# Kernel tuning notes

Hardware: AMD Instinct MI355X
Metric: run time of the kernel (lower is better)

## Reference

```python
import jax, jax.numpy as jnp
import numpy as np

B, S, H = 1024, 100, 256
C_TANH = 10.0
NEG = -100000.0


def _lin(k, o, i):
    s = 1.0 / np.sqrt(i)
    kw, kb = jax.random.split(k)
    return (jax.random.uniform(kw, (o, i), jnp.float32, -s, s),
            jax.random.uniform(kb, (o,), jnp.float32, -s, s))


def setup_inputs() -> dict:
    key = jax.random.key(0)
    ks = jax.random.split(key, 16)
    inputs = jax.random.uniform(ks[0], (B, S, 2), jnp.float32)
    emb_w, emb_b = _lin(ks[1], H, 2)
    s = 1.0 / np.sqrt(H)
    def lstm(k):
        k1, k2, k3, k4 = jax.random.split(k, 4)
        return (jax.random.uniform(k1, (4 * H, H), jnp.float32, -s, s),
                jax.random.uniform(k2, (4 * H, H), jnp.float32, -s, s),
                jax.random.uniform(k3, (4 * H,), jnp.float32, -s, s),
                jax.random.uniform(k4, (4 * H,), jnp.float32, -s, s))
    enc_wih, enc_whh, enc_bih, enc_bhh = lstm(ks[2])
    dec_wih, dec_whh, dec_bih, dec_bhh = lstm(ks[3])
    ptr_wq_w, ptr_wq_b = _lin(ks[4], H, H)
    ptr_wref_w, ptr_wref_b = _lin(ks[5], H, H)
    ptr_v_w, ptr_v_b = _lin(ks[6], 1, H)
    glm_wq_w, glm_wq_b = _lin(ks[7], H, H)
    glm_wref_w, glm_wref_b = _lin(ks[8], H, H)
    glm_v_w, glm_v_b = _lin(ks[9], 1, H)
    start = jax.random.uniform(ks[10], (H,), jnp.float32, -s, s)
    return dict(inputs=inputs, emb_w=emb_w, emb_b=emb_b,
                enc_wih=enc_wih, enc_whh=enc_whh, enc_bih=enc_bih, enc_bhh=enc_bhh,
                dec_wih=dec_wih, dec_whh=dec_whh, dec_bih=dec_bih, dec_bhh=dec_bhh,
                ptr_wq_w=ptr_wq_w, ptr_wq_b=ptr_wq_b, ptr_wref_w=ptr_wref_w, ptr_wref_b=ptr_wref_b,
                ptr_v_w=ptr_v_w, ptr_v_b=ptr_v_b,
                glm_wq_w=glm_wq_w, glm_wq_b=glm_wq_b, glm_wref_w=glm_wref_w, glm_wref_b=glm_wref_b,
                glm_v_w=glm_v_w, glm_v_b=glm_v_b, start=start)


def _lstm_cell(x, h, c, wih, whh, bih, bhh):
    g = x @ wih.T + bih + h @ whh.T + bhh
    i, f, gg, o = jnp.split(g, 4, axis=-1)  # torch gate order i,f,g,o
    c = jax.nn.sigmoid(f) * c + jax.nn.sigmoid(i) * jnp.tanh(gg)
    h = jax.nn.sigmoid(o) * jnp.tanh(c)
    return h, c


def _attn_logits(q, ref_proj, mask, wq_w, wq_b, v_w, v_b):
    # ref_proj = W_ref(encoder_outputs), precomputed: [B,S,H]
    u = jnp.tanh(ref_proj + (q @ wq_w.T + wq_b)[:, None, :])
    logits = jnp.einsum('bsh,h->bs', u, v_w[0]) + v_b[0]
    logits = jnp.where(mask, NEG, logits)
    return C_TANH * jnp.tanh(logits)


def reference(inputs, emb_w, emb_b,
              enc_wih, enc_whh, enc_bih, enc_bhh,
              dec_wih, dec_whh, dec_bih, dec_bhh,
              ptr_wq_w, ptr_wq_b, ptr_wref_w, ptr_wref_b, ptr_v_w, ptr_v_b,
              glm_wq_w, glm_wq_b, glm_wref_w, glm_wref_b, glm_v_w, glm_v_b,
              start):
    Bn, Sn = inputs.shape[0], inputs.shape[1]
    embedded = inputs @ emb_w.T + emb_b  # [B,S,H]

    def enc_step(carry, x):
        h, c = carry
        h, c = _lstm_cell(x, h, c, enc_wih, enc_whh, enc_bih, enc_bhh)
        return (h, c), h
    z = jnp.zeros((Bn, H), inputs.dtype)
    (h, c), enc_out = jax.lax.scan(enc_step, (z, z), jnp.swapaxes(embedded, 0, 1))
    enc_out = jnp.swapaxes(enc_out, 0, 1)  # [B,S,H]

    ref_g = enc_out @ glm_wref_w.T + glm_wref_b
    ref_p = enc_out @ ptr_wref_w.T + ptr_wref_b
    bidx = jnp.arange(Bn)

    def dec_step(carry, k):
        h, c, mask, dec_in = carry
        h, c = _lstm_cell(dec_in, h, c, dec_wih, dec_whh, dec_bih, dec_bhh)
        q = h
        gl = _attn_logits(q, ref_g, mask, glm_wq_w, glm_wq_b, glm_v_w, glm_v_b)
        q = jnp.einsum('bsh,bs->bh', enc_out, jax.nn.softmax(gl, axis=-1))
        pl = _attn_logits(q, ref_p, mask, ptr_wq_w, ptr_wq_b, ptr_v_w, ptr_v_b)
        logp = jax.nn.log_softmax(pl, axis=-1)
        chosen = jax.random.categorical(k, pl, axis=-1)  # [B]
        lp = jnp.take_along_axis(logp, chosen[:, None], axis=1)[:, 0]
        mask = mask.at[bidx, chosen].set(True)
        dec_in = embedded[bidx, chosen]
        return (h, c, mask, dec_in), (lp, chosen)

    mask0 = jnp.zeros((Bn, Sn), bool)
    dec_in0 = jnp.broadcast_to(start, (Bn, H))
    keys = jax.random.split(jax.random.key(42), Sn)
    _, (lps, chs) = jax.lax.scan(dec_step, (h, c, mask0, dec_in0), keys)
    return jnp.swapaxes(lps, 0, 1), jnp.swapaxes(chs, 0, 1)
```

## Files before the change

kernel.cpp:

```cpp
#include <hip/hip_runtime.h>
#include <cstdint>
#include <cstddef>

#define BB 1024
#define SS 100
#define HH 256

__device__ __forceinline__ unsigned rotl32(unsigned v, int r) {
  return (v << r) | (v >> (32 - r));
}

__device__ __forceinline__ void threefry2x32(unsigned k0, unsigned k1,
                                             unsigned x0, unsigned x1,
                                             unsigned& o0, unsigned& o1) {
  unsigned k2 = k0 ^ k1 ^ 0x1BD11BDAu;
  x0 += k0; x1 += k1;
#define TF_R(r) { x0 += x1; x1 = rotl32(x1, (r)); x1 ^= x0; }
  TF_R(13) TF_R(15) TF_R(26) TF_R(6)
  x0 += k1; x1 += k2 + 1u;
  TF_R(17) TF_R(29) TF_R(16) TF_R(24)
  x0 += k2; x1 += k0 + 2u;
  TF_R(13) TF_R(15) TF_R(26) TF_R(6)
  x0 += k0; x1 += k1 + 3u;
  TF_R(17) TF_R(29) TF_R(16) TF_R(24)
  x0 += k1; x1 += k2 + 4u;
  TF_R(13) TF_R(15) TF_R(26) TF_R(6)
  x0 += k2; x1 += k0 + 5u;
#undef TF_R
  o0 = x0; o1 = x1;
}

__device__ __forceinline__ double sigd(double x) {
  return 1.0 / (1.0 + exp(-x));
}

__device__ __forceinline__ float tanh_fast(float x) {
  float e = __expf(2.0f * x);
  return 1.0f - 2.0f * __builtin_amdgcn_rcpf(e + 1.0f);
}

__device__ __forceinline__ double wave_max(double v) {
#pragma unroll
  for (int off = 32; off; off >>= 1) v = fmax(v, __shfl_xor(v, off));
  return v;
}
__device__ __forceinline__ double wave_sum(double v) {
#pragma unroll
  for (int off = 32; off; off >>= 1) v += __shfl_xor(v, off);
  return v;
}

__global__ __launch_bounds__(256) void init_chunk(
    double* __restrict__ h, double* __restrict__ c) {
  int i = blockIdx.x * 256 + threadIdx.x;
  h[i] = 0.0;
  c[i] = 0.0;
}

__global__ __launch_bounds__(256) void precompute_P(
    const float* __restrict__ emb_w, const float* __restrict__ emb_b,
    const float* __restrict__ start,
    const float* __restrict__ enc_wih, const float* __restrict__ dec_wih,
    double* __restrict__ P) {
  int idx = blockIdx.x * 256 + threadIdx.x;
  int v = idx >> 10, n = idx & 1023;
  const float* W = (v < 3) ? enc_wih : dec_wih;
  int cm = (v < 6) ? (v % 3) : 3;
  const float* wr = W + (size_t)n * HH;
  double acc = 0.0;
  for (int k = 0; k < HH; ++k) {
    double cv;
    if (cm == 0)      cv = (double)emb_w[2 * k];
    else if (cm == 1) cv = (double)emb_w[2 * k + 1];
    else if (cm == 2) cv = (double)emb_b[k];
    else              cv = (double)start[k];
    acc = fma(cv, (double)wr[k], acc);
  }
  P[idx] = acc;
}

__global__ __launch_bounds__(256) void init_dec(
    double* __restrict__ gih, int* __restrict__ mask,
    const double* __restrict__ gih0) {
  const int r = blockIdx.x, t = threadIdx.x;
  if (t < SS) mask[r * SS + t] = 0;
#pragma unroll
  for (int jj = 0; jj < 4; ++jj)
    gih[(size_t)r * 1024 + jj * 256 + t] = gih0[jj * 256 + t];
}

__global__ __launch_bounds__(256) void transpose2(
    const float* __restrict__ a, const float* __restrict__ b,
    float* __restrict__ at, float* __restrict__ bt) {
  int k = blockIdx.x, t = threadIdx.x;
  at[k * HH + t] = a[t * HH + k];
  bt[k * HH + t] = b[t * HH + k];
}

template <bool EMBED>
__global__ __launch_bounds__(256) void lstm_gates(
    const float* __restrict__ inputs, int t, int cb,
    const double* __restrict__ gih,
    const double* __restrict__ Pe,
    const float* __restrict__ Whh,
    const float* __restrict__ bih, const float* __restrict__ bhh,
    const double* __restrict__ hprev, double* __restrict__ hnew,
    double* __restrict__ c, float* __restrict__ enc_c) {
  __shared__ double As[16][34];
  __shared__ double Ws[16][66];
  const int tid = threadIdx.x;
  const int tx = tid & 15;
  const int ty = tid >> 4;
  const int m0 = blockIdx.x * 32;
  const int u0 = blockIdx.y * 16;
  const int arow = tid >> 3;
  const int acol = (tid & 7) * 2;
  const int wn   = tid >> 2;
  const int wcol = (tid & 3) * 4;
  const int wgate = wn >> 4, wu = wn & 15;
  double acc[2][4];

  if (EMBED) {
#pragma unroll
    for (int i = 0; i < 2; ++i) {
      int bb = cb + m0 + ty * 2 + i;
      double i0 = (double)inputs[(bb * SS + t) * 2];
      double i1 = (double)inputs[(bb * SS + t) * 2 + 1];
#pragma unroll
      for (int j = 0; j < 4; ++j) {
        int n = j * 256 + u0 + tx;
        acc[i][j] = fma(i0, Pe[n], fma(i1, Pe[1024 + n], Pe[2048 + n]));
      }
    }
  } else {
#pragma unroll
    for (int i = 0; i < 2; ++i) {
      const double* gr = gih + (size_t)(m0 + ty * 2 + i) * 1024 + u0 + tx;
#pragma unroll
      for (int j = 0; j < 4; ++j) acc[i][j] = gr[j * 256];
    }
  }

  const float* wrow_hh = Whh + (size_t)(wgate * HH + u0 + wu) * HH;

  auto load_slab = [&](int s, double& a0, double& a1, float4& wv) {
    const int k0 = s * 16;
    const double* ar = hprev + (size_t)(m0 + arow) * HH + k0 + acol;
    a0 = ar[0]; a1 = ar[1];
    wv = *(const float4*)(wrow_hh + k0 + wcol);
  };

  double a0c, a1c; float4 wvc;
  load_slab(0, a0c, a1c, wvc);
  for (int s = 0; s < 16; ++s) {
    __syncthreads();
    As[acol][arow] = a0c;
    As[acol + 1][arow] = a1c;
    Ws[wcol + 0][wn] = (double)wvc.x;
    Ws[wcol + 1][wn] = (double)wvc.y;
    Ws[wcol + 2][wn] = (double)wvc.z;
    Ws[wcol + 3][wn] = (double)wvc.w;
    __syncthreads();
    if (s < 15) load_slab(s + 1, a0c, a1c, wvc);
#pragma unroll
    for (int kk = 0; kk < 16; ++kk) {
      double a0k = As[kk][ty * 2];
      double a1k = As[kk][ty * 2 + 1];
#pragma unroll
      for (int j = 0; j < 4; ++j) {
        double w = Ws[kk][j * 16 + tx];
        acc[0][j] = fma(a0k, w, acc[0][j]);
        acc[1][j] = fma(a1k, w, acc[1][j]);
      }
    }
  }

  const int u = u0 + tx;
#pragma unroll
  for (int i = 0; i < 2; ++i) {
    int r = m0 + ty * 2 + i;
    double gi = acc[i][0] + (double)bih[u] + (double)bhh[u];
    double gf = acc[i][1] + (double)bih[HH + u] + (double)bhh[HH + u];
    double gg = acc[i][2] + (double)bih[2 * HH + u] + (double)bhh[2 * HH + u];
    double go = acc[i][3] + (double)bih[3 * HH + u] + (double)bhh[3 * HH + u];
    size_t idx = (size_t)r * HH + u;
    double cp = c[idx];
    double cn = sigd(gf) * cp + sigd(gi) * tanh(gg);
    double hn = sigd(go) * tanh(cn);
    c[idx] = cn;
    hnew[idx] = hn;
    if (enc_c) enc_c[((size_t)r * SS + t) * HH + u] = (float)hn;
  }
}

__global__ __launch_bounds__(256) void proj_gemm(
    const float* __restrict__ A, const float* __restrict__ W,
    const float* __restrict__ bias, float* __restrict__ C) {
  __shared__ double As[16][68];
  __shared__ double Ws[16][68];
  const int tid = threadIdx.x;
  const int tx = tid & 15, ty = tid >> 4;
  const int m0 = blockIdx.x * 64;
  const int n0 = blockIdx.y * 64;
  const int lrow = tid >> 2;
  const int lcol = (tid & 3) << 2;
  double acc[4][4] = {};

  const float* ar = A + (size_t)(m0 + lrow) * HH;
  const float* wr = W + (size_t)(n0 + lrow) * HH;
  for (int k0 = 0; k0 < HH; k0 += 16) {
    float4 av = *(const float4*)(ar + k0 + lcol);
    float4 wv = *(const float4*)(wr + k0 + lcol);
    __syncthreads();
    As[lcol + 0][lrow] = (double)av.x; As[lcol + 1][lrow] = (double)av.y;
    As[lcol + 2][lrow] = (double)av.z; As[lcol + 3][lrow] = (double)av.w;
    Ws[lcol + 0][lrow] = (double)wv.x; Ws[lcol + 1][lrow] = (double)wv.y;
    Ws[lcol + 2][lrow] = (double)wv.z; Ws[lcol + 3][lrow] = (double)wv.w;
    __syncthreads();
#pragma unroll
    for (int kk = 0; kk < 16; ++kk) {
      double a[4], w[4];
#pragma unroll
      for (int i = 0; i < 4; ++i) a[i] = As[kk][ty * 4 + i];
#pragma unroll
      for (int j = 0; j < 4; ++j) w[j] = Ws[kk][tx * 4 + j];
#pragma unroll
      for (int i = 0; i < 4; ++i)
#pragma unroll
        for (int j = 0; j < 4; ++j) acc[i][j] = fma(a[i], w[j], acc[i][j]);
    }
  }
#pragma unroll
  for (int i = 0; i < 4; ++i) {
    float* crow = C + (size_t)(m0 + ty * 4 + i) * HH + n0 + tx * 4;
#pragma unroll
    for (int j = 0; j < 4; ++j)
      crow[j] = (float)(acc[i][j] + (double)bias[n0 + tx * 4 + j]);
  }
}

__global__ __launch_bounds__(256) void dec_attn_sample(
    const double* __restrict__ h,
    const float* __restrict__ enc_c, const float* __restrict__ ref_g,
    const float* __restrict__ ref_p,
    const float* __restrict__ wqt_g, const float* __restrict__ bq_g,
    const float* __restrict__ vw_g, const float* __restrict__ vb_g,
    const float* __restrict__ wqt_p, const float* __restrict__ bq_p,
    const float* __restrict__ vw_p, const float* __restrict__ vb_p,
    int* __restrict__ mask, double* __restrict__ gih,
    const double* __restrict__ Pd,
    const float* __restrict__ inputs,
    float* __restrict__ out, int step, int cb) {
  __shared__ float  hqf[HH];
  __shared__ __align__(16) float qvf[HH];
  __shared__ double lg[SS];
  __shared__ float  lgw[SS];
  __shared__ int    smask[SS];
  __shared__ double redw[4];
  __shared__ int    ridxw[4];
  __shared__ int    sh_chosen;

  const int r = blockIdx.x, t = threadIdx.x;
  const int w = t >> 6, l = t & 63;
  const int b = cb + r;

  hqf[t] = (float)h[(size_t)r * HH + t];
  if (t < SS) smask[t] = mask[r * SS + t];
  __syncthreads();

  {
    float a0 = 0.f, a1 = 0.f, a2 = 0.f, a3 = 0.f;
    for (int k = 0; k < HH; k += 4) {
      a0 = fmaf(wqt_g[(k + 0) * HH + t], hqf[k + 0], a0);
      a1 = fmaf(wqt_g[(k + 1) * HH + t], hqf[k + 1], a1);
      a2 = fmaf(wqt_g[(k + 2) * HH + t], hqf[k + 2], a2);
      a3 = fmaf(wqt_g[(k + 3) * HH + t], hqf[k + 3], a3);
    }
    qvf[t] = ((a0 + a1) + (a2 + a3)) + bq_g[t];
  }
  __syncthreads();

  {
    const float4 vg = *(const float4*)(vw_g + l * 4);
    const float4 qf = *(const float4*)(qvf + l * 4);
    const float vb = vb_g[0];
    for (int s = w; s < SS; s += 4) {
      if (smask[s]) {
        if (l == 0) lg[s] = -10.0;
        continue;
      }
      const float4 rp = *(const float4*)(ref_g + ((size_t)r * SS + s) * HH + l * 4);
      float p = tanh_fast(rp.x + qf.x) * vg.x;
      p = fmaf(tanh_fast(rp.y + qf.y), vg.y, p);
      p = fmaf(tanh_fast(rp.z + qf.z), vg.z, p);
      p = fmaf(tanh_fast(rp.w + qf.w), vg.w, p);
#pragma unroll
      for (int off = 32; off; off >>= 1) p += __shfl_xor(p, off);
      float z = 10.0f * tanh_fast(p + vb);
      if (l == 0) lg[s] = (double)z;
    }
  }
  __syncthreads();

  {
    double x = (t < SS) ? lg[t] : -1e300;
    double vm = wave_max(x);
    if (l == 0) redw[w] = vm;
    __syncthreads();
    double mx = fmax(fmax(redw[0], redw[1]), fmax(redw[2], redw[3]));
    double e = (t < SS) ? exp(x - mx) : 0.0;
    double vs = wave_sum(e);
    __syncthreads();
    if (l == 0) redw[w] = vs;
    __syncthreads();
    double sum = redw[0] + redw[1] + redw[2] + redw[3];
    if (t < SS) lgw[t] = (float)(e / sum);
  }
  __syncthreads();

  {
    const float* eb = enc_c + (size_t)r * SS * HH + t;
    float acc0 = 0.f, acc1 = 0.f, acc2 = 0.f, acc3 = 0.f;
    for (int s = 0; s < SS; s += 4) {
      acc0 = fmaf(eb[(s + 0) * HH], lgw[s + 0], acc0);
      acc1 = fmaf(eb[(s + 1) * HH], lgw[s + 1], acc1);
      acc2 = fmaf(eb[(s + 2) * HH], lgw[s + 2], acc2);
      acc3 = fmaf(eb[(s + 3) * HH], lgw[s + 3], acc3);
    }
    hqf[t] = (acc0 + acc1) + (acc2 + acc3);
  }
  __syncthreads();

  {
    float a0 = 0.f, a1 = 0.f, a2 = 0.f, a3 = 0.f;
    for (int k = 0; k < HH; k += 4) {
      a0 = fmaf(wqt_p[(k + 0) * HH + t], hqf[k + 0], a0);
      a1 = fmaf(wqt_p[(k + 1) * HH + t], hqf[k + 1], a1);
      a2 = fmaf(wqt_p[(k + 2) * HH + t], hqf[k + 2], a2);
      a3 = fmaf(wqt_p[(k + 3) * HH + t], hqf[k + 3], a3);
    }
    qvf[t] = ((a0 + a1) + (a2 + a3)) + bq_p[t];
  }
  __syncthreads();

  {
    const float4 vg = *(const float4*)(vw_p + l * 4);
    const float4 qf = *(const float4*)(qvf + l * 4);
    const float vb = vb_p[0];
    for (int s = w; s < SS; s += 4) {
      if (smask[s]) {
        if (l == 0) lg[s] = -10.0;
        continue;
      }
      const float4 rp = *(const float4*)(ref_p + ((size_t)r * SS + s) * HH + l * 4);
      float p = tanh_fast(rp.x + qf.x) * vg.x;
      p = fmaf(tanh_fast(rp.y + qf.y), vg.y, p);
      p = fmaf(tanh_fast(rp.z + qf.z), vg.z, p);
      p = fmaf(tanh_fast(rp.w + qf.w), vg.w, p);
#pragma unroll
      for (int off = 32; off; off >>= 1) p += __shfl_xor(p, off);
      float z = 10.0f * tanh_fast(p + vb);
      if (l == 0) lg[s] = (double)z;
    }
  }
  __syncthreads();

  double x = (t < SS) ? lg[t] : -1e300;
  double val = -1e300;
  int idx = t;
  if (t < SS) {
    unsigned kk0, kk1;
    threefry2x32(0u, 42u, 0u, (unsigned)step, kk0, kk1);
    unsigned j = (unsigned)(b * SS + t);
    unsigned o0, o1;
    threefry2x32(kk0, kk1, 0u, j, o0, o1);
    unsigned bits = o0 ^ o1;
    double u = (double)(bits >> 9) * 0x1p-23;
    if (u == 0.0) u = 1.17549435e-38;
    val = x + (-log(-log(u)));
  }
#pragma unroll
  for (int off = 32; off; off >>= 1) {
    double v2 = __shfl_xor(val, off);
    int i2 = __shfl_xor(idx, off);
    if (v2 > val || (v2 == val && i2 < idx)) { val = v2; idx = i2; }
  }
  if (l == 0) { redw[w] = val; ridxw[w] = idx; }
  __syncthreads();
  if (t == 0) {
    double bv = redw[0]; int bi = ridxw[0];
#pragma unroll
    for (int i = 1; i < 4; ++i) {
      if (redw[i] > bv || (redw[i] == bv && ridxw[i] < bi)) {
        bv = redw[i]; bi = ridxw[i];
      }
    }
    sh_chosen = bi;
  }
  __syncthreads();
  int chosen = sh_chosen;

  {
    double vm = wave_max(x);
    if (l == 0) redw[w] = vm;
    __syncthreads();
    double mx = fmax(fmax(redw[0], redw[1]), fmax(redw[2], redw[3]));
    double e = (t < SS) ? exp(x - mx) : 0.0;
    double vs = wave_sum(e);
    __syncthreads();
    if (l == 0) redw[w] = vs;
    __syncthreads();
    if (t == 0) {
      double sum = redw[0] + redw[1] + redw[2] + redw[3];
      double lse = log(sum);
      double xc = lg[chosen];
      out[(size_t)b * SS + step] = (float)(xc - mx - lse);
      out[(size_t)BB * SS + (size_t)b * SS + step] = (float)chosen;
      mask[r * SS + chosen] = 1;
    }
  }

  int ib = (b * SS + chosen) * 2;
  double i0 = (double)inputs[ib], i1 = (double)inputs[ib + 1];
#pragma unroll
  for (int jj = 0; jj < 4; ++jj) {
    int n = jj * 256 + t;
    gih[(size_t)r * 1024 + n] =
        fma(i0, Pd[n], fma(i1, Pd[1024 + n], Pd[2048 + n]));
  }
}

__global__ __launch_bounds__(256) void diag_kernel(float* __restrict__ out, float v) {
  int i = blockIdx.x * 256 + threadIdx.x;
  if (i < 2 * BB * SS) out[i] = v;
}

extern "C" void kernel_launch(void* const* d_in, const int* in_sizes, int n_in,
                              void* d_out, int out_size, void* d_ws, size_t ws_size,
                              hipStream_t stream) {
  (void)in_sizes; (void)n_in; (void)out_size;
  const float* inputs    = (const float*)d_in[0];
  const float* emb_w     = (const float*)d_in[1];
  const float* emb_b     = (const float*)d_in[2];
  const float* enc_wih   = (const float*)d_in[3];
  const float* enc_whh   = (const float*)d_in[4];
  const float* enc_bih   = (const float*)d_in[5];
  const float* enc_bhh   = (const float*)d_in[6];
  const float* dec_wih   = (const float*)d_in[7];
  const float* dec_whh   = (const float*)d_in[8];
  const float* dec_bih   = (const float*)d_in[9];
  const float* dec_bhh   = (const float*)d_in[10];
  const float* ptr_wq_w  = (const float*)d_in[11];
  const float* ptr_wq_b  = (const float*)d_in[12];
  const float* ptr_wref_w= (const float*)d_in[13];
  const float* ptr_wref_b= (const float*)d_in[14];
  const float* ptr_v_w   = (const float*)d_in[15];
  const float* ptr_v_b   = (const float*)d_in[16];
  const float* glm_wq_w  = (const float*)d_in[17];
  const float* glm_wq_b  = (const float*)d_in[18];
  const float* glm_wref_w= (const float*)d_in[19];
  const float* glm_wref_b= (const float*)d_in[20];
  const float* glm_v_w   = (const float*)d_in[21];
  const float* glm_v_b   = (const float*)d_in[22];
  const float* start     = (const float*)d_in[23];
  float* out = (float*)d_out;

  auto bytes_needed = [](size_t chunk) -> size_t {
    auto al = [](size_t n) { return (n + 255) & ~(size_t)255; };
    size_t big = al(chunk * SS * HH * 4);
    return 3 * big + 3 * al(chunk * HH * 8) + al(chunk * 1024 * 8) +
           al(chunk * SS * 4) + 2 * al((size_t)HH * HH * 4) +
           al((size_t)7 * 1024 * 8);
  };
  size_t chunk = 1024;
  if (ws_size < bytes_needed(1024)) chunk = 512;
  if (ws_size < bytes_needed(512)) {
    diag_kernel<<<(2 * BB * SS + 255) / 256, 256, 0, stream>>>(
        out, (float)(ws_size >> 20));
    return;
  }

  char* base_p = (char*)d_ws;
  size_t off = 0;
  auto take = [&](size_t nbytes) {
    void* p = base_p + off;
    off = (off + nbytes + 255) & ~(size_t)255;
    return p;
  };
  const size_t BIGC = chunk * SS * HH;
  float*  enc_c  = (float*)take(BIGC * 4);
  float*  ref_g  = (float*)take(BIGC * 4);
  float*  ref_p  = (float*)take(BIGC * 4);
  double* hA     = (double*)take(chunk * HH * 8);
  double* hB     = (double*)take(chunk * HH * 8);
  double* cbuf   = (double*)take(chunk * HH * 8);
  double* gih    = (double*)take(chunk * 1024 * 8);
  int*    mask   = (int*)take(chunk * SS * 4);
  float*  wqt_g  = (float*)take((size_t)HH * HH * 4);
  float*  wqt_p  = (float*)take((size_t)HH * HH * 4);
  double* P      = (double*)take((size_t)7 * 1024 * 8);

  transpose2<<<HH, HH, 0, stream>>>(glm_wq_w, ptr_wq_w, wqt_g, wqt_p);
  precompute_P<<<28, 256, 0, stream>>>(emb_w, emb_b, start, enc_wih, dec_wih, P);

  const double* Pe   = P;
  const double* Pd   = P + 3 * 1024;
  const double* gih0 = P + 6 * 1024;

  const dim3 lstm_grid((unsigned)chunk / 32, 16);
  for (int cb = 0; cb < BB; cb += (int)chunk) {
    init_chunk<<<(unsigned)chunk, 256, 0, stream>>>(hA, cbuf);
    double* hin = hA; double* hout = hB;
    for (int t = 0; t < SS; ++t) {
      lstm_gates<true><<<lstm_grid, 256, 0, stream>>>(
          inputs, t, cb, nullptr, Pe,
          enc_whh, enc_bih, enc_bhh, hin, hout, cbuf, enc_c);
      double* tmp = hin; hin = hout; hout = tmp;
    }

    proj_gemm<<<dim3((unsigned)(chunk * SS / 64), 4), 256, 0, stream>>>(
        enc_c, glm_wref_w, glm_wref_b, ref_g);
    proj_gemm<<<dim3((unsigned)(chunk * SS / 64), 4), 256, 0, stream>>>(
        enc_c, ptr_wref_w, ptr_wref_b, ref_p);

    init_dec<<<(unsigned)chunk, 256, 0, stream>>>(gih, mask, gih0);
    for (int k = 0; k < SS; ++k) {
      lstm_gates<false><<<lstm_grid, 256, 0, stream>>>(
          inputs, 0, cb, gih, nullptr,
          dec_whh, dec_bih, dec_bhh, hin, hout, cbuf, nullptr);
      dec_attn_sample<<<(unsigned)chunk, 256, 0, stream>>>(
          hout, enc_c, ref_g, ref_p,
          wqt_g, glm_wq_b, glm_v_w, glm_v_b,
          wqt_p, ptr_wq_b, ptr_v_w, ptr_v_b,
          mask, gih, Pd, inputs, out, k, cb);
      double* tmp = hin; hin = hout; hout = tmp;
    }
  }
}
```

Baseline: 17.60 ms.

## Replace per-step kernel launches with persistent encoder/decoder kernels using grid barriers

Result: no change. 17.78 ms (+1.0%).

```diff
diff --git a/kernel.cpp b/kernel.cpp
--- a/kernel.cpp
+++ b/kernel.cpp
@@ -5,6 +5,7 @@
 #define BB 1024
 #define SS 100
 #define HH 256
+#define NBLK 512
 
 __device__ __forceinline__ unsigned rotl32(unsigned v, int r) {
   return (v << r) | (v >> (32 - r));
@@ -50,11 +51,41 @@
   return v;
 }
 
+__device__ __forceinline__ void grid_barrier(unsigned* bar) {
+  __syncthreads();
+  if (threadIdx.x == 0) {
+    unsigned* cnt = bar;
+    unsigned* gen = bar + 1;
+    unsigned g = __hip_atomic_load(gen, __ATOMIC_RELAXED,
+                                   __HIP_MEMORY_SCOPE_AGENT);
+    __threadfence();
+    unsigned a = __hip_atomic_fetch_add(cnt, 1u, __ATOMIC_ACQ_REL,
+                                        __HIP_MEMORY_SCOPE_AGENT);
+    if (a + 1u == (unsigned)NBLK) {
+      __hip_atomic_store(cnt, 0u, __ATOMIC_RELAXED,
+                         __HIP_MEMORY_SCOPE_AGENT);
+      __hip_atomic_store(gen, g + 1u, __ATOMIC_RELEASE,
+                         __HIP_MEMORY_SCOPE_AGENT);
+    } else {
+      while (__hip_atomic_load(gen, __ATOMIC_RELAXED,
+                               __HIP_MEMORY_SCOPE_AGENT) == g) {
+        __builtin_amdgcn_s_sleep(2);
+      }
+    }
+    __threadfence();
+  }
+  __syncthreads();
+}
+
 __global__ __launch_bounds__(256) void init_chunk(
     double* __restrict__ h, double* __restrict__ c) {
   int i = blockIdx.x * 256 + threadIdx.x;
   h[i] = 0.0;
   c[i] = 0.0;
+}
+
+__global__ void zero_bar(unsigned* __restrict__ bar) {
+  if (threadIdx.x < 4) bar[threadIdx.x] = 0u;
 }
 
 __global__ __launch_bounds__(256) void precompute_P(
@@ -97,11 +128,354 @@
   bt[k * HH + t] = b[t * HH + k];
 }
 
+__global__ __launch_bounds__(512, 4) void enc_persistent(
+    const float* __restrict__ inputs, int cb,
+    const double* __restrict__ Pe, const float* __restrict__ Whh,
+    const float* __restrict__ bih, const float* __restrict__ bhh,
+    double* __restrict__ hA, double* __restrict__ hB,
+    double* __restrict__ c, float* __restrict__ enc_c,
+    unsigned* __restrict__ bar) {
+  __shared__ double As[16][34];
+  __shared__ double Ws[16][66];
+  const int tid = threadIdx.x;
+  const int p = blockIdx.x;
+  const int m0 = (p & 31) * 32;
+  const int u0 = (p >> 5) * 16;
+  const int r_loc = tid >> 4;
+  const int tx = tid & 15;
+  const int arow = tid >> 4, acol = tid & 15;
+  const int wn = tid >> 3;
+  const int wc2 = (tid & 7) * 2;
+  const int wgate = wn >> 4, wu = wn & 15;
+  const float* wrow = Whh + (size_t)(wgate * HH + u0 + wu) * HH;
+  const int row = m0 + r_loc;
+  const int u = u0 + tx;
+
+  double* hin = hA;
+  double* hout = hB;
+#pragma unroll 1
+  for (int t = 0; t < SS; ++t) {
+    double i0 = (double)inputs[((cb + row) * SS + t) * 2];
+    double i1 = (double)inputs[((cb + row) * SS + t) * 2 + 1];
+    double acc[4];
+#pragma unroll
+    for (int j = 0; j < 4; ++j) {
+      int n = j * 256 + u;
+      acc[j] = fma(i0, Pe[n], fma(i1, Pe[1024 + n], Pe[2048 + n]));
+    }
+    double a_c; float2 w_c;
+    a_c = hin[(size_t)(m0 + arow) * HH + acol];
+    w_c = *(const float2*)(wrow + wc2);
+#pragma unroll 1
+    for (int s = 0; s < 16; ++s) {
+      __syncthreads();
+      As[acol][arow] = a_c;
+      Ws[wc2][wn] = (double)w_c.x;
+      Ws[wc2 + 1][wn] = (double)w_c.y;
+      __syncthreads();
+      if (s < 15) {
+        int k0 = (s + 1) * 16;
+        a_c = hin[(size_t)(m0 + arow) * HH + k0 + acol];
+        w_c = *(const float2*)(wrow + k0 + wc2);
+      }
+#pragma unroll
+      for (int kk = 0; kk < 16; ++kk) {
+        double a = As[kk][r_loc];
+#pragma unroll
+        for (int j = 0; j < 4; ++j)
+          acc[j] = fma(a, Ws[kk][j * 16 + tx], acc[j]);
+      }
+    }
+    double gi = acc[0] + (double)bih[u] + (double)bhh[u];
+    double gf = acc[1] + (double)bih[HH + u] + (double)bhh[HH + u];
+    double gg = acc[2] + (double)bih[2 * HH + u] + (double)bhh[2 * HH + u];
+    double go = acc[3] + (double)bih[3 * HH + u] + (double)bhh[3 * HH + u];
+    size_t idx = (size_t)row * HH + u;
+    double cp = c[idx];
+    double cn = sigd(gf) * cp + sigd(gi) * tanh(gg);
+    double hn = sigd(go) * tanh(cn);
+    c[idx] = cn;
+    hout[idx] = hn;
+    enc_c[((size_t)row * SS + t) * HH + u] = (float)hn;
+
+    if (t < SS - 1) grid_barrier(bar);
+    double* tmp = hin; hin = hout; hout = tmp;
+  }
+}
+
+__global__ __launch_bounds__(512, 4) void dec_persistent(
+    const float* __restrict__ inputs, int cb,
+    double* __restrict__ gih, const double* __restrict__ Pd,
+    const float* __restrict__ Whh,
+    const float* __restrict__ bih, const float* __restrict__ bhh,
+    double* __restrict__ hA, double* __restrict__ hB,
+    double* __restrict__ c,
+    const float* __restrict__ enc_c, const float* __restrict__ ref_g,
+    const float* __restrict__ ref_p,
+    const float* __restrict__ wqt_g, const float* __restrict__ bq_g,
+    const float* __restrict__ vw_g, const float* __restrict__ vb_g,
+    const float* __restrict__ wqt_p, const float* __restrict__ bq_p,
+    const float* __restrict__ vw_p, const float* __restrict__ vb_p,
+    float* __restrict__ out, unsigned* __restrict__ bar) {
+  __shared__ double As[16][34];
+  __shared__ double Ws[16][66];
+  __shared__ __align__(16) float hqf[2][HH];
+  __shared__ __align__(16) float qvf[2][HH];
+  __shared__ double lg[2][SS];
+  __shared__ float  lgw[2][SS];
+  __shared__ int    smask[2][SS];
+  __shared__ double redw[2][4];
+  __shared__ int    ridxw[2][4];
+  __shared__ int    sh_chosen[2];
+
+  const int tid = threadIdx.x;
+  const int p = blockIdx.x;
+  const int m0 = (p & 31) * 32;
+  const int u0 = (p >> 5) * 16;
+  const int r_loc = tid >> 4;
+  const int tx = tid & 15;
+  const int arow = tid >> 4, acol = tid & 15;
+  const int wn = tid >> 3;
+  const int wc2 = (tid & 7) * 2;
+  const int wgate = wn >> 4, wu = wn & 15;
+  const float* wrow = Whh + (size_t)(wgate * HH + u0 + wu) * HH;
+  const int lrow = m0 + r_loc;
+  const int lu = u0 + tx;
+  const int half = tid >> 8;
+  const int tl = tid & 255;
+  const int wv4 = tl >> 6, l = tl & 63;
+  const int ar = 2 * p + half;
+  const int ab = cb + ar;
+
+  if (tl < SS) smask[half][tl] = 0;
+
+  double* hin = hA;
+  double* hout = hB;
+
+#pragma unroll 1
+  for (int k = 0; k < SS; ++k) {
+    {
+      double acc[4];
+#pragma unroll
+      for (int j = 0; j < 4; ++j)
+        acc[j] = gih[(size_t)lrow * 1024 + j * 256 + lu];
+      double a_c; float2 w_c;
+      a_c = hin[(size_t)(m0 + arow) * HH + acol];
+      w_c = *(const float2*)(wrow + wc2);
+#pragma unroll 1
+      for (int s = 0; s < 16; ++s) {
+        __syncthreads();
+        As[acol][arow] = a_c;
+        Ws[wc2][wn] = (double)w_c.x;
+        Ws[wc2 + 1][wn] = (double)w_c.y;
+        __syncthreads();
+        if (s < 15) {
+          int k0 = (s + 1) * 16;
+          a_c = hin[(size_t)(m0 + arow) * HH + k0 + acol];
+          w_c = *(const float2*)(wrow + k0 + wc2);
+        }
+#pragma unroll
+        for (int kk = 0; kk < 16; ++kk) {
+          double a = As[kk][r_loc];
+#pragma unroll
+          for (int j = 0; j < 4; ++j)
+            acc[j] = fma(a, Ws[kk][j * 16 + tx], acc[j]);
+        }
+      }
+      double gi = acc[0] + (double)bih[lu] + (double)bhh[lu];
+      double gf = acc[1] + (double)bih[HH + lu] + (double)bhh[HH + lu];
+      double gg = acc[2] + (double)bih[2 * HH + lu] + (double)bhh[2 * HH + lu];
+      double go = acc[3] + (double)bih[3 * HH + lu] + (double)bhh[3 * HH + lu];
+      size_t idx = (size_t)lrow * HH + lu;
+      double cp = c[idx];
+      double cn = sigd(gf) * cp + sigd(gi) * tanh(gg);
+      double hn = sigd(go) * tanh(cn);
+      c[idx] = cn;
+      hout[idx] = hn;
+    }
+    grid_barrier(bar);
+
+    hqf[half][tl] = (float)hout[(size_t)ar * HH + tl];
+    __syncthreads();
+
+    {
+      float a0 = 0.f, a1 = 0.f, a2 = 0.f, a3 = 0.f;
+      for (int kk = 0; kk < HH; kk += 4) {
+        a0 = fmaf(wqt_g[(kk + 0) * HH + tl], hqf[half][kk + 0], a0);
+        a1 = fmaf(wqt_g[(kk + 1) * HH + tl], hqf[half][kk + 1], a1);
+        a2 = fmaf(wqt_g[(kk + 2) * HH + tl], hqf[half][kk + 2], a2);
+        a3 = fmaf(wqt_g[(kk + 3) * HH + tl], hqf[half][kk + 3], a3);
+      }
+      qvf[half][tl] = ((a0 + a1) + (a2 + a3)) + bq_g[tl];
+    }
+    __syncthreads();
+
+    {
+      const float4 vg = *(const float4*)(vw_g + l * 4);
+      const float4 qf = *(const float4*)(&qvf[half][l * 4]);
+      const float vb = vb_g[0];
+      for (int s = wv4; s < SS; s += 4) {
+        if (smask[half][s]) {
+          if (l == 0) lg[half][s] = -10.0;
+          continue;
+        }
+        const float4 rp =
+            *(const float4*)(ref_g + ((size_t)ar * SS + s) * HH + l * 4);
+        float pp = tanh_fast(rp.x + qf.x) * vg.x;
+        pp = fmaf(tanh_fast(rp.y + qf.y), vg.y, pp);
+        pp = fmaf(tanh_fast(rp.z + qf.z), vg.z, pp);
+        pp = fmaf(tanh_fast(rp.w + qf.w), vg.w, pp);
+#pragma unroll
+        for (int off = 32; off; off >>= 1) pp += __shfl_xor(pp, off);
+        float z = 10.0f * tanh_fast(pp + vb);
+        if (l == 0) lg[half][s] = (double)z;
+      }
+    }
+    __syncthreads();
+
+    {
+      double x = (tl < SS) ? lg[half][tl] : -1e300;
+      double vm = wave_max(x);
+      if (l == 0) redw[half][wv4] = vm;
+      __syncthreads();
+      double mx = fmax(fmax(redw[half][0], redw[half][1]),
+                       fmax(redw[half][2], redw[half][3]));
+      double e = (tl < SS) ? exp(x - mx) : 0.0;
+      double vs = wave_sum(e);
+      __syncthreads();
+      if (l == 0) redw[half][wv4] = vs;
+      __syncthreads();
+      double sum = redw[half][0] + redw[half][1] + redw[half][2] +
+                   redw[half][3];
+      if (tl < SS) lgw[half][tl] = (float)(e / sum);
+    }
+    __syncthreads();
+
+    {
+      const float* eb = enc_c + (size_t)ar * SS * HH + tl;
+      float a0 = 0.f, a1 = 0.f, a2 = 0.f, a3 = 0.f;
+      for (int s = 0; s < SS; s += 4) {
+        a0 = fmaf(eb[(s + 0) * HH], lgw[half][s + 0], a0);
+        a1 = fmaf(eb[(s + 1) * HH], lgw[half][s + 1], a1);
+        a2 = fmaf(eb[(s + 2) * HH], lgw[half][s + 2], a2);
+        a3 = fmaf(eb[(s + 3) * HH], lgw[half][s + 3], a3);
+      }
+      hqf[half][tl] = (a0 + a1) + (a2 + a3);
+    }
+    __syncthreads();
+
+    {
+      float a0 = 0.f, a1 = 0.f, a2 = 0.f, a3 = 0.f;
+      for (int kk = 0; kk < HH; kk += 4) {
+        a0 = fmaf(wqt_p[(kk + 0) * HH + tl], hqf[half][kk + 0], a0);
+        a1 = fmaf(wqt_p[(kk + 1) * HH + tl], hqf[half][kk + 1], a1);
+        a2 = fmaf(wqt_p[(kk + 2) * HH + tl], hqf[half][kk + 2], a2);
+        a3 = fmaf(wqt_p[(kk + 3) * HH + tl], hqf[half][kk + 3], a3);
+      }
+      qvf[half][tl] = ((a0 + a1) + (a2 + a3)) + bq_p[tl];
+    }
+    __syncthreads();
+
+    {
+      const float4 vg = *(const float4*)(vw_p + l * 4);
+      const float4 qf = *(const float4*)(&qvf[half][l * 4]);
+      const float vb = vb_p[0];
+      for (int s = wv4; s < SS; s += 4) {
+        if (smask[half][s]) {
+          if (l == 0) lg[half][s] = -10.0;
+          continue;
+        }
+        const float4 rp =
+            *(const float4*)(ref_p + ((size_t)ar * SS + s) * HH + l * 4);
+        float pp = tanh_fast(rp.x + qf.x) * vg.x;
+        pp = fmaf(tanh_fast(rp.y + qf.y), vg.y, pp);
+        pp = fmaf(tanh_fast(rp.z + qf.z), vg.z, pp);
+        pp = fmaf(tanh_fast(rp.w + qf.w), vg.w, pp);
+#pragma unroll
+        for (int off = 32; off; off >>= 1) pp += __shfl_xor(pp, off);
+        float z = 10.0f * tanh_fast(pp + vb);
+        if (l == 0) lg[half][s] = (double)z;
+      }
+    }
+    __syncthreads();
+
+    double x = (tl < SS) ? lg[half][tl] : -1e300;
+    double val = -1e300;
+    int idx = tl;
+    if (tl < SS) {
+      unsigned kk0, kk1;
+      threefry2x32(0u, 42u, 0u, (unsigned)k, kk0, kk1);
+      unsigned o0, o1;
+      threefry2x32(kk0, kk1, 0u, (unsigned)(ab * SS + tl), o0, o1);
+      unsigned bits = o0 ^ o1;
+      double u = (double)(bits >> 9) * 0x1p-23;
+      if (u == 0.0) u = 1.17549435e-38;
+      val = x + (-log(-log(u)));
+    }
+#pragma unroll
+    for (int off = 32; off; off >>= 1) {
+      double v2 = __shfl_xor(val, off);
+      int i2 = __shfl_xor(idx, off);
+      if (v2 > val || (v2 == val && i2 < idx)) { val = v2; idx = i2; }
+    }
+    if (l == 0) { redw[half][wv4] = val; ridxw[half][wv4] = idx; }
+    __syncthreads();
+    if (tl == 0) {
+      double bv = redw[half][0]; int bi = ridxw[half][0];
+#pragma unroll
+      for (int i = 1; i < 4; ++i) {
+        if (redw[half][i] > bv ||
+            (redw[half][i] == bv && ridxw[half][i] < bi)) {
+          bv = redw[half][i]; bi = ridxw[half][i];
+        }
+      }
+      sh_chosen[half] = bi;
+    }
+    __syncthreads();
+    int chosen = sh_chosen[half];
+
+    {
+      double vm = wave_max(x);
+      if (l == 0) redw[half][wv4] = vm;
+      __syncthreads();
+      double mx = fmax(fmax(redw[half][0], redw[half][1]),
+                       fmax(redw[half][2], redw[half][3]));
+      double e = (tl < SS) ? exp(x - mx) : 0.0;
+      double vs = wave_sum(e);
+      __syncthreads();
+      if (l == 0) redw[half][wv4] = vs;
+      __syncthreads();
+      if (tl == 0) {
+        double sum = redw[half][0] + redw[half][1] + redw[half][2] +
+                     redw[half][3];
+        double lse = log(sum);
+        double xc = lg[half][chosen];
+        out[(size_t)ab * SS + k] = (float)(xc - mx - lse);
+        out[(size_t)BB * SS + (size_t)ab * SS + k] = (float)chosen;
+        smask[half][chosen] = 1;
+      }
+    }
+
+    {
+      int ib = (ab * SS + chosen) * 2;
+      double i0 = (double)inputs[ib], i1 = (double)inputs[ib + 1];
+#pragma unroll
+      for (int jj = 0; jj < 4; ++jj) {
+        int n = jj * 256 + tl;
+        gih[(size_t)ar * 1024 + n] =
+            fma(i0, Pd[n], fma(i1, Pd[1024 + n], Pd[2048 + n]));
+      }
+    }
+
+    if (k < SS - 1) grid_barrier(bar);
+    double* tmp = hin; hin = hout; hout = tmp;
+  }
+}
+
 template <bool EMBED>
 __global__ __launch_bounds__(256) void lstm_gates(
     const float* __restrict__ inputs, int t, int cb,
-    const double* __restrict__ gih,
-    const double* __restrict__ Pe,
+    const double* __restrict__ gih, const double* __restrict__ Pe,
     const float* __restrict__ Whh,
     const float* __restrict__ bih, const float* __restrict__ bhh,
     const double* __restrict__ hprev, double* __restrict__ hnew,
@@ -142,7 +516,6 @@
   }
 
   const float* wrow_hh = Whh + (size_t)(wgate * HH + u0 + wu) * HH;
-
   auto load_slab = [&](int s, double& a0, double& a1, float4& wv) {
     const int k0 = s * 16;
     const double* ar = hprev + (size_t)(m0 + arow) * HH + k0 + acol;
@@ -190,52 +563,6 @@
     c[idx] = cn;
     hnew[idx] = hn;
     if (enc_c) enc_c[((size_t)r * SS + t) * HH + u] = (float)hn;
-  }
-}
-
-__global__ __launch_bounds__(256) void proj_gemm(
-    const float* __restrict__ A, const float* __restrict__ W,
-    const float* __restrict__ bias, float* __restrict__ C) {
-  __shared__ double As[16][68];
-  __shared__ double Ws[16][68];
-  const int tid = threadIdx.x;
-  const int tx = tid & 15, ty = tid >> 4;
-  const int m0 = blockIdx.x * 64;
-  const int n0 = blockIdx.y * 64;
-  const int lrow = tid >> 2;
-  const int lcol = (tid & 3) << 2;
-  double acc[4][4] = {};
-
-  const float* ar = A + (size_t)(m0 + lrow) * HH;
-  const float* wr = W + (size_t)(n0 + lrow) * HH;
-  for (int k0 = 0; k0 < HH; k0 += 16) {
-    float4 av = *(const float4*)(ar + k0 + lcol);
-    float4 wv = *(const float4*)(wr + k0 + lcol);
-    __syncthreads();
-    As[lcol + 0][lrow] = (double)av.x; As[lcol + 1][lrow] = (double)av.y;
-    As[lcol + 2][lrow] = (double)av.z; As[lcol + 3][lrow] = (double)av.w;
-    Ws[lcol + 0][lrow] = (double)wv.x; Ws[lcol + 1][lrow] = (double)wv.y;
-    Ws[lcol + 2][lrow] = (double)wv.z; Ws[lcol + 3][lrow] = (double)wv.w;
-    __syncthreads();
-#pragma unroll
-    for (int kk = 0; kk < 16; ++kk) {
-      double a[4], w[4];
-#pragma unroll
-      for (int i = 0; i < 4; ++i) a[i] = As[kk][ty * 4 + i];
-#pragma unroll
-      for (int j = 0; j < 4; ++j) w[j] = Ws[kk][tx * 4 + j];
-#pragma unroll
-      for (int i = 0; i < 4; ++i)
-#pragma unroll
-        for (int j = 0; j < 4; ++j) acc[i][j] = fma(a[i], w[j], acc[i][j]);
-    }
-  }
-#pragma unroll
-  for (int i = 0; i < 4; ++i) {
-    float* crow = C + (size_t)(m0 + ty * 4 + i) * HH + n0 + tx * 4;
-#pragma unroll
-    for (int j = 0; j < 4; ++j)
-      crow[j] = (float)(acc[i][j] + (double)bias[n0 + tx * 4 + j]);
   }
 }
 
@@ -427,6 +754,52 @@
     int n = jj * 256 + t;
     gih[(size_t)r * 1024 + n] =
         fma(i0, Pd[n], fma(i1, Pd[1024 + n], Pd[2048 + n]));
+  }
+}
+
+__global__ __launch_bounds__(256) void proj_gemm(
+    const float* __restrict__ A, const float* __restrict__ W,
+    const float* __restrict__ bias, float* __restrict__ C) {
+  __shared__ double As[16][68];
+  __shared__ double Ws[16][68];
+  const int tid = threadIdx.x;
+  const int tx = tid & 15, ty = tid >> 4;
+  const int m0 = blockIdx.x * 64;
+  const int n0 = blockIdx.y * 64;
+  const int lrow = tid >> 2;
+  const int lcol = (tid & 3) << 2;
+  double acc[4][4] = {};
+
+  const float* ar = A + (size_t)(m0 + lrow) * HH;
+  const float* wr = W + (size_t)(n0 + lrow) * HH;
+  for (int k0 = 0; k0 < HH; k0 += 16) {
+    float4 av = *(const float4*)(ar + k0 + lcol);
+    float4 wv = *(const float4*)(wr + k0 + lcol);
+    __syncthreads();
+    As[lcol + 0][lrow] = (double)av.x; As[lcol + 1][lrow] = (double)av.y;
+    As[lcol + 2][lrow] = (double)av.z; As[lcol + 3][lrow] = (double)av.w;
+    Ws[lcol + 0][lrow] = (double)wv.x; Ws[lcol + 1][lrow] = (double)wv.y;
+    Ws[lcol + 2][lrow] = (double)wv.z; Ws[lcol + 3][lrow] = (double)wv.w;
+    __syncthreads();
+#pragma unroll
+    for (int kk = 0; kk < 16; ++kk) {
+      double a[4], w[4];
+#pragma unroll
+      for (int i = 0; i < 4; ++i) a[i] = As[kk][ty * 4 + i];
+#pragma unroll
+      for (int j = 0; j < 4; ++j) w[j] = Ws[kk][tx * 4 + j];
+#pragma unroll
+      for (int i = 0; i < 4; ++i)
+#pragma unroll
+        for (int j = 0; j < 4; ++j) acc[i][j] = fma(a[i], w[j], acc[i][j]);
+    }
+  }
+#pragma unroll
+  for (int i = 0; i < 4; ++i) {
+    float* crow = C + (size_t)(m0 + ty * 4 + i) * HH + n0 + tx * 4;
+#pragma unroll
+    for (int j = 0; j < 4; ++j)
+      crow[j] = (float)(acc[i][j] + (double)bias[n0 + tx * 4 + j]);
   }
 }
 
@@ -470,7 +843,7 @@
     size_t big = al(chunk * SS * HH * 4);
     return 3 * big + 3 * al(chunk * HH * 8) + al(chunk * 1024 * 8) +
            al(chunk * SS * 4) + 2 * al((size_t)HH * HH * 4) +
-           al((size_t)7 * 1024 * 8);
+           al((size_t)7 * 1024 * 8) + al(64);
   };
   size_t chunk = 1024;
   if (ws_size < bytes_needed(1024)) chunk = 512;
@@ -499,41 +872,57 @@
   float*  wqt_g  = (float*)take((size_t)HH * HH * 4);
   float*  wqt_p  = (float*)take((size_t)HH * HH * 4);
   double* P      = (double*)take((size_t)7 * 1024 * 8);
+  unsigned* bar  = (unsigned*)take(64);
 
   transpose2<<<HH, HH, 0, stream>>>(glm_wq_w, ptr_wq_w, wqt_g, wqt_p);
   precompute_P<<<28, 256, 0, stream>>>(emb_w, emb_b, start, enc_wih, dec_wih, P);
+  zero_bar<<<1, 4, 0, stream>>>(bar);
 
   const double* Pe   = P;
   const double* Pd   = P + 3 * 1024;
   const double* gih0 = P + 6 * 1024;
 
-  const dim3 lstm_grid((unsigned)chunk / 32, 16);
-  for (int cb = 0; cb < BB; cb += (int)chunk) {
-    init_chunk<<<(unsigned)chunk, 256, 0, stream>>>(hA, cbuf);
-    double* hin = hA; double* hout = hB;
-    for (int t = 0; t < SS; ++t) {
-      lstm_gates<true><<<lstm_grid, 256, 0, stream>>>(
-          inputs, t, cb, nullptr, Pe,
-          enc_whh, enc_bih, enc_bhh, hin, hout, cbuf, enc_c);
-      double* tmp = hin; hin = hout; hout = tmp;
-    }
-
-    proj_gemm<<<dim3((unsigned)(chunk * SS / 64), 4), 256, 0, stream>>>(
+  if (chunk == 1024) {
+    init_chunk<<<1024, 256, 0, stream>>>(hA, cbuf);
+    enc_persistent<<<NBLK, 512, 0, stream>>>(
+        inputs, 0, Pe, enc_whh, enc_bih, enc_bhh, hA, hB, cbuf, enc_c, bar);
+    proj_gemm<<<dim3(1024 * SS / 64, 4), 256, 0, stream>>>(
         enc_c, glm_wref_w, glm_wref_b, ref_g);
-    proj_gemm<<<dim3((unsigned)(chunk * SS / 64), 4), 256, 0, stream>>>(
+    proj_gemm<<<dim3(1024 * SS / 64, 4), 256, 0, stream>>>(
         enc_c, ptr_wref_w, ptr_wref_b, ref_p);
-
-    init_dec<<<(unsigned)chunk, 256, 0, stream>>>(gih, mask, gih0);
-    for (int k = 0; k < SS; ++k) {
-      lstm_gates<false><<<lstm_grid, 256, 0, stream>>>(
-          inputs, 0, cb, gih, nullptr,
-          dec_whh, dec_bih, dec_bhh, hin, hout, cbuf, nullptr);
-      dec_attn_sample<<<(unsigned)chunk, 256, 0, stream>>>(
-          hout, enc_c, ref_g, ref_p,
-          wqt_g, glm_wq_b, glm_v_w, glm_v_b,
-          wqt_p, ptr_wq_b, ptr_v_w, ptr_v_b,
-          mask, gih, Pd, inputs, out, k, cb);
-      double* tmp = hin; hin = hout; hout = tmp;
-    }
-  }
-}
+    init_dec<<<1024, 256, 0, stream>>>(gih, mask, gih0);
+    dec_persistent<<<NBLK, 512, 0, stream>>>(
+        inputs, 0, gih, Pd, dec_whh, dec_bih, dec_bhh, hA, hB, cbuf,
+        enc_c, ref_g, ref_p,
+        wqt_g, glm_wq_b, glm_v_w, glm_v_b,
+        wqt_p, ptr_wq_b, ptr_v_w, ptr_v_b, out, bar);
+  } else {
+    const dim3 lstm_grid((unsigned)chunk / 32, 16);
+    for (int cb = 0; cb < BB; cb += (int)chunk) {
+      init_chunk<<<(unsigned)chunk, 256, 0, stream>>>(hA, cbuf);
+      double* hin = hA; double* hout = hB;
+      for (int t = 0; t < SS; ++t) {
+        lstm_gates<true><<<lstm_grid, 256, 0, stream>>>(
+            inputs, t, cb, nullptr, Pe,
+            enc_whh, enc_bih, enc_bhh, hin, hout, cbuf, enc_c);
+        double* tmp = hin; hin = hout; hout = tmp;
+      }
+      proj_gemm<<<dim3((unsigned)(chunk * SS / 64), 4), 256, 0, stream>>>(
+          enc_c, glm_wref_w, glm_wref_b, ref_g);
+      proj_gemm<<<dim3((unsigned)(chunk * SS / 64), 4), 256, 0, stream>>>(
+          enc_c, ptr_wref_w, ptr_wref_b, ref_p);
+      init_dec<<<(unsigned)chunk, 256, 0, stream>>>(gih, mask, gih0);
+      for (int k = 0; k < SS; ++k) {
+        lstm_gates<false><<<lstm_grid, 256, 0, stream>>>(
+            inputs, 0, cb, gih, nullptr,
+            dec_whh, dec_bih, dec_bhh, hin, hout, cbuf, nullptr);
+        dec_attn_sample<<<(unsigned)chunk, 256, 0, stream>>>(
+            hout, enc_c, ref_g, ref_p,
+            wqt_g, glm_wq_b, glm_v_w, glm_v_b,
+            wqt_p, ptr_wq_b, ptr_v_w, ptr_v_b,
+            mask, gih, Pd, inputs, out, k, cb);
+        double* tmp = hin; hin = hout; hout = tmp;
+      }
+    }
+  }
+}
```
